# Kernel optimization log

Measured on AMD Instinct MI355X. Metric: run time of the kernel, lower is better.

The kernel has to match this reference:

```python
import jax, jax.numpy as jnp
import numpy as np

ITERS = 20
EPS = 1e-6

def setup_inputs() -> dict:
    key = jax.random.key(0)
    logits = jax.random.normal(key, (128, 64, 64, 64), dtype=jnp.float32)
    return {"logits": logits}

def reference(logits) -> jnp.ndarray:
    # Per-(H,W) matrix: stabilized exp over rows, then 20 Sinkhorn iterations.
    x = logits.astype(jnp.float32)
    # row-wise max (over W, last axis), matching tl.max(x, axis=1)
    x = jnp.exp(x - jnp.max(x, axis=-1, keepdims=True))

    def body(i, x):
        row_sum = jnp.sum(x, axis=-1, keepdims=True)   # sum over W
        x = x / (row_sum + EPS)
        col_sum = jnp.sum(x, axis=-2, keepdims=True)   # sum over H
        x = x / (col_sum + EPS)
        return x

    x = jax.lax.fori_loop(0, ITERS, body, x)
    return x
```

## Files before the change

### kernel.cpp

```cpp
#include <hip/hip_runtime.h>


static constexpr int   kIters = 20;
static constexpr float kEps   = 1e-6f;

__device__ __forceinline__ float RLf(float x, int l) {
    return __int_as_float(__builtin_amdgcn_readlane(__float_as_int(x), l));
}

__global__ __launch_bounds__(256, 4) void sinkhorn64_2m4(const float* __restrict__ in,
                                                         float* __restrict__ out) {
    __shared__ float xb0[2][2][64];
    __shared__ float xb1[2][2][64];
    const int tid  = threadIdx.x;
    const int wid  = tid >> 6;
    const int p    = wid >> 1;
    const int h    = wid & 1;
    const int lane = tid & 63;
    const int c    = (lane + 32 * h) & 63;
    const long m   = (long)blockIdx.x * 2 + p;
    const float* __restrict__ A = in  + m * 4096;
    float* __restrict__ O       = out + m * 4096;

    float cK[32];
#pragma unroll
    for (int i = 0; i < 32; ++i) cK[i] = A[((32 * h + i) << 6) + lane];

    float rK[32];
#pragma unroll
    for (int k4 = 0; k4 < 8; ++k4) {
        const float4 f = *reinterpret_cast<const float4*>(A + (lane << 6) + 32 * h + (k4 << 2));
        rK[4 * k4 + 0] = f.x; rK[4 * k4 + 1] = f.y;
        rK[4 * k4 + 2] = f.z; rK[4 * k4 + 3] = f.w;
    }

    float pm = rK[0];
#pragma unroll
    for (int k = 1; k < 32; ++k) pm = fmaxf(pm, rK[k]);
    xb0[p][h][lane] = pm;
    __syncthreads();
    const float mx  = fmaxf(pm, xb0[p][1 - h][lane]);
    const float mxr = fmaxf(xb0[p][0][c], xb0[p][1][c]);

#pragma unroll
    for (int k = 0; k < 32; ++k) rK[k] = __expf(rK[k] - mx);
#pragma unroll
    for (int i = 0; i < 32; ++i) cK[i] = __expf(cK[i] - RLf(mxr, i));

    float ur = 1.0f, vr = 1.0f;

#pragma unroll 1
    for (int it = 0; it < kIters; ++it) {
        float a0 = 0.f, a1 = 0.f, a2 = 0.f, a3 = 0.f;
#pragma unroll
        for (int k = 0; k < 32; k += 4) {
            a0 = fmaf(RLf(vr, k + 0), rK[k + 0], a0);
            a1 = fmaf(RLf(vr, k + 1), rK[k + 1], a1);
            a2 = fmaf(RLf(vr, k + 2), rK[k + 2], a2);
            a3 = fmaf(RLf(vr, k + 3), rK[k + 3], a3);
        }
        xb1[p][h][lane] = (a0 + a1) + (a2 + a3);
        __syncthreads();
        const float w = xb1[p][0][c] + xb1[p][1][c];
        ur = ur * __builtin_amdgcn_rcpf(fmaf(ur, w, kEps));

        float b0 = 0.f, b1 = 0.f, b2 = 0.f, b3 = 0.f;
#pragma unroll
        for (int i = 0; i < 32; i += 4) {
            b0 = fmaf(RLf(ur, i + 0), cK[i + 0], b0);
            b1 = fmaf(RLf(ur, i + 1), cK[i + 1], b1);
            b2 = fmaf(RLf(ur, i + 2), cK[i + 2], b2);
            b3 = fmaf(RLf(ur, i + 3), cK[i + 3], b3);
        }
        xb0[p][h][lane] = (b0 + b1) + (b2 + b3);
        __syncthreads();
        const float t = xb0[p][0][c] + xb0[p][1][c];
        vr = vr * __builtin_amdgcn_rcpf(fmaf(vr, t, kEps));
    }

    xb1[p][h][lane] = vr;
    __syncthreads();
    const float vfin = xb1[p][0][lane];

#pragma unroll
    for (int i = 0; i < 32; ++i) {
        O[((32 * h + i) << 6) + lane] = RLf(ur, i) * cK[i] * vfin;
    }
}

extern "C" void kernel_launch(void* const* d_in, const int* in_sizes, int n_in,
                              void* d_out, int out_size, void* d_ws, size_t ws_size,
                              hipStream_t stream) {
    const float* in = (const float*)d_in[0];
    float* out      = (float*)d_out;
    sinkhorn64_2m4<<<4096, 256, 0, stream>>>(in, out);
}
```

Before: 87.91 us.

## Store Sinkhorn kernel and scaling vectors in packed fp16 using fdot2

Converts the exponentiated matrix (row and column copies) and the u/v scaling vectors to packed half2 and computes the matrix-vector sums with v_dot2 fp16 instructions that accumulate in fp32. This halves register use for the kernel matrix and the number of readlane and FMA instructions per iteration. It also drops the minBlocks launch bound so occupancy is chosen by register use. The cost is fp16 precision on the matrix entries and on the iterated scalings, which may exceed the accuracy tolerance, and fp16 can underflow for small exp values.

Measured after the change: 117.7 us. 1.34x slower.

```diff
diff --git a/kernel.cpp b/kernel.cpp
--- a/kernel.cpp
+++ b/kernel.cpp
@@ -4,12 +4,22 @@
 static constexpr int   kIters = 20;
 static constexpr float kEps   = 1e-6f;
 
+typedef _Float16 h2 __attribute__((ext_vector_type(2)));
+
 __device__ __forceinline__ float RLf(float x, int l) {
     return __int_as_float(__builtin_amdgcn_readlane(__float_as_int(x), l));
 }
+__device__ __forceinline__ h2 RLh2(h2 x, int l) {
+    int bits;
+    __builtin_memcpy(&bits, &x, 4);
+    int r = __builtin_amdgcn_readlane(bits, l);
+    h2 out;
+    __builtin_memcpy(&out, &r, 4);
+    return out;
+}
 
-__global__ __launch_bounds__(256, 4) void sinkhorn64_2m4(const float* __restrict__ in,
-                                                         float* __restrict__ out) {
+__global__ __launch_bounds__(256) void sinkhorn64_h2(const float* __restrict__ in,
+                                                     float* __restrict__ out) {
     __shared__ float xb0[2][2][64];
     __shared__ float xb1[2][2][64];
     const int tid  = threadIdx.x;
@@ -17,74 +27,100 @@
     const int p    = wid >> 1;
     const int h    = wid & 1;
     const int lane = tid & 63;
-    const int c    = (lane + 32 * h) & 63;
+    const int pl   = lane & 31;
     const long m   = (long)blockIdx.x * 2 + p;
     const float* __restrict__ A = in  + m * 4096;
     float* __restrict__ O       = out + m * 4096;
 
-    float cK[32];
-#pragma unroll
-    for (int i = 0; i < 32; ++i) cK[i] = A[((32 * h + i) << 6) + lane];
-
-    float rK[32];
+    float rKf[32];
 #pragma unroll
     for (int k4 = 0; k4 < 8; ++k4) {
         const float4 f = *reinterpret_cast<const float4*>(A + (lane << 6) + 32 * h + (k4 << 2));
-        rK[4 * k4 + 0] = f.x; rK[4 * k4 + 1] = f.y;
-        rK[4 * k4 + 2] = f.z; rK[4 * k4 + 3] = f.w;
+        rKf[4 * k4 + 0] = f.x; rKf[4 * k4 + 1] = f.y;
+        rKf[4 * k4 + 2] = f.z; rKf[4 * k4 + 3] = f.w;
+    }
+    float pm = rKf[0];
+#pragma unroll
+    for (int k = 1; k < 32; ++k) pm = fmaxf(pm, rKf[k]);
+    xb0[p][h][lane] = pm;
+    __syncthreads();
+    const float mx = fmaxf(pm, xb0[p][1 - h][lane]);
+
+    h2 rH[16];
+#pragma unroll
+    for (int t = 0; t < 16; ++t) {
+        rH[t].x = (_Float16)__expf(rKf[2 * t + 0] - mx);
+        rH[t].y = (_Float16)__expf(rKf[2 * t + 1] - mx);
     }
 
-    float pm = rK[0];
+    h2 cH[16];
 #pragma unroll
-    for (int k = 1; k < 32; ++k) pm = fmaxf(pm, rK[k]);
-    xb0[p][h][lane] = pm;
-    __syncthreads();
-    const float mx  = fmaxf(pm, xb0[p][1 - h][lane]);
-    const float mxr = fmaxf(xb0[p][0][c], xb0[p][1][c]);
+    for (int t = 0; t < 16; ++t) {
+        const float x0 = A[((32 * h + 2 * t + 0) << 6) + lane];
+        const float x1 = A[((32 * h + 2 * t + 1) << 6) + lane];
+        cH[t].x = (_Float16)__expf(x0 - RLf(mx, 32 * h + 2 * t + 0));
+        cH[t].y = (_Float16)__expf(x1 - RLf(mx, 32 * h + 2 * t + 1));
+    }
 
-#pragma unroll
-    for (int k = 0; k < 32; ++k) rK[k] = __expf(rK[k] - mx);
-#pragma unroll
-    for (int i = 0; i < 32; ++i) cK[i] = __expf(cK[i] - RLf(mxr, i));
-
-    float ur = 1.0f, vr = 1.0f;
+    h2 up; up.x = (_Float16)1.0f; up.y = (_Float16)1.0f;
+    h2 vp = up;
+    const int rlbase = 16 * h;
 
 #pragma unroll 1
     for (int it = 0; it < kIters; ++it) {
-        float a0 = 0.f, a1 = 0.f, a2 = 0.f, a3 = 0.f;
+        {
+            float a0 = 0.f, a1 = 0.f, a2 = 0.f, a3 = 0.f;
 #pragma unroll
-        for (int k = 0; k < 32; k += 4) {
-            a0 = fmaf(RLf(vr, k + 0), rK[k + 0], a0);
-            a1 = fmaf(RLf(vr, k + 1), rK[k + 1], a1);
-            a2 = fmaf(RLf(vr, k + 2), rK[k + 2], a2);
-            a3 = fmaf(RLf(vr, k + 3), rK[k + 3], a3);
+            for (int t = 0; t < 16; t += 4) {
+                a0 = __builtin_amdgcn_fdot2(rH[t + 0], RLh2(vp, rlbase + t + 0), a0, false);
+                a1 = __builtin_amdgcn_fdot2(rH[t + 1], RLh2(vp, rlbase + t + 1), a1, false);
+                a2 = __builtin_amdgcn_fdot2(rH[t + 2], RLh2(vp, rlbase + t + 2), a2, false);
+                a3 = __builtin_amdgcn_fdot2(rH[t + 3], RLh2(vp, rlbase + t + 3), a3, false);
+            }
+            xb1[p][h][lane] = (a0 + a1) + (a2 + a3);
         }
-        xb1[p][h][lane] = (a0 + a1) + (a2 + a3);
         __syncthreads();
-        const float w = xb1[p][0][c] + xb1[p][1][c];
-        ur = ur * __builtin_amdgcn_rcpf(fmaf(ur, w, kEps));
+        {
+            const float2 a = *reinterpret_cast<const float2*>(&xb1[p][0][2 * pl]);
+            const float2 b = *reinterpret_cast<const float2*>(&xb1[p][1][2 * pl]);
+            float u0 = (float)up.x, u1 = (float)up.y;
+            u0 = u0 * __builtin_amdgcn_rcpf(fmaf(u0, a.x + b.x, kEps));
+            u1 = u1 * __builtin_amdgcn_rcpf(fmaf(u1, a.y + b.y, kEps));
+            up.x = (_Float16)u0; up.y = (_Float16)u1;
+        }
 
-        float b0 = 0.f, b1 = 0.f, b2 = 0.f, b3 = 0.f;
+        {
+            float a0 = 0.f, a1 = 0.f, a2 = 0.f, a3 = 0.f;
 #pragma unroll
-        for (int i = 0; i < 32; i += 4) {
-            b0 = fmaf(RLf(ur, i + 0), cK[i + 0], b0);
-            b1 = fmaf(RLf(ur, i + 1), cK[i + 1], b1);
-            b2 = fmaf(RLf(ur, i + 2), cK[i + 2], b2);
-            b3 = fmaf(RLf(ur, i + 3), cK[i + 3], b3);
+            for (int t = 0; t < 16; t += 4) {
+                a0 = __builtin_amdgcn_fdot2(cH[t + 0], RLh2(up, rlbase + t + 0), a0, false);
+                a1 = __builtin_amdgcn_fdot2(cH[t + 1], RLh2(up, rlbase + t + 1), a1, false);
+                a2 = __builtin_amdgcn_fdot2(cH[t + 2], RLh2(up, rlbase + t + 2), a2, false);
+                a3 = __builtin_amdgcn_fdot2(cH[t + 3], RLh2(up, rlbase + t + 3), a3, false);
+            }
+            xb0[p][h][lane] = (a0 + a1) + (a2 + a3);
         }
-        xb0[p][h][lane] = (b0 + b1) + (b2 + b3);
         __syncthreads();
-        const float t = xb0[p][0][c] + xb0[p][1][c];
-        vr = vr * __builtin_amdgcn_rcpf(fmaf(vr, t, kEps));
+        {
+            const float2 a = *reinterpret_cast<const float2*>(&xb0[p][0][2 * pl]);
+            const float2 b = *reinterpret_cast<const float2*>(&xb0[p][1][2 * pl]);
+            float v0 = (float)vp.x, v1 = (float)vp.y;
+            v0 = v0 * __builtin_amdgcn_rcpf(fmaf(v0, a.x + b.x, kEps));
+            v1 = v1 * __builtin_amdgcn_rcpf(fmaf(v1, a.y + b.y, kEps));
+            vp.x = (_Float16)v0; vp.y = (_Float16)v1;
+        }
     }
 
-    xb1[p][h][lane] = vr;
     __syncthreads();
-    const float vfin = xb1[p][0][lane];
+    reinterpret_cast<h2*>(&xb0[p][0][0])[pl] = vp;
+    __syncthreads();
+    const float vf = (float)reinterpret_cast<const _Float16*>(&xb0[p][0][0])[lane];
 
 #pragma unroll
-    for (int i = 0; i < 32; ++i) {
-        O[((32 * h + i) << 6) + lane] = RLf(ur, i) * cK[i] * vfin;
+    for (int t = 0; t < 16; ++t) {
+        const h2 u2 = RLh2(up, rlbase + t);
+        O[((32 * h + 2 * t + 0) << 6) + lane] = (float)u2.x * (float)cH[t].x * vf;
+        O[((32 * h + 2 * t + 1) << 6) + lane] = (float)u2.y * (float)cH[t].y * vf;
     }
 }
 
@@ -93,5 +129,5 @@
                               hipStream_t stream) {
     const float* in = (const float*)d_in[0];
     float* out      = (float*)d_out;
-    sinkhorn64_2m4<<<4096, 256, 0, stream>>>(in, out);
+    sinkhorn64_h2<<<4096, 256, 0, stream>>>(in, out);
 }
```

## Hand-write Sinkhorn loop in inline asm with packed FP32 FMAs

Applied to the files above, without the earlier changes.

Replaces the compiler-generated 20-iteration Sinkhorn loop with an inline assembly block. It broadcasts scaling factors through v_readlane into SGPR pairs and accumulates with v_pk_fma_f32, which handles two matrix entries per instruction and halves the FMA instruction count. The two partial sums are kept as float2 pairs in LDS and reduced after the barrier with four ds_read_b32. The risks are hardcoded SGPR clobbers, hand-inserted s_nop hazard padding, and dropping the occupancy hint in launch_bounds.

Measured after the change: 93.02 us. +5.8%, slower.

```diff
diff --git a/kernel.cpp b/kernel.cpp
--- a/kernel.cpp
+++ b/kernel.cpp
@@ -1,17 +1,17 @@
 #include <hip/hip_runtime.h>
 
 
-static constexpr int   kIters = 20;
-static constexpr float kEps   = 1e-6f;
+static constexpr float kEps = 1e-6f;
 
 __device__ __forceinline__ float RLf(float x, int l) {
     return __int_as_float(__builtin_amdgcn_readlane(__float_as_int(x), l));
 }
 
-__global__ __launch_bounds__(256, 4) void sinkhorn64_2m4(const float* __restrict__ in,
-                                                         float* __restrict__ out) {
-    __shared__ float xb0[2][2][64];
-    __shared__ float xb1[2][2][64];
+__global__ __launch_bounds__(256) void sinkhorn64_asm2(const float* __restrict__ in,
+                                                       float* __restrict__ out) {
+    __shared__ float2 xw[2][2][64];
+    __shared__ float2 xt[2][2][64];
+    __shared__ float  mbuf[2][2][64];
     const int tid  = threadIdx.x;
     const int wid  = tid >> 6;
     const int p    = wid >> 1;
@@ -22,69 +22,179 @@
     const float* __restrict__ A = in  + m * 4096;
     float* __restrict__ O       = out + m * 4096;
 
-    float cK[32];
-#pragma unroll
-    for (int i = 0; i < 32; ++i) cK[i] = A[((32 * h + i) << 6) + lane];
-
-    float rK[32];
+    float cKf[32];
+#pragma unroll
+    for (int i = 0; i < 32; ++i) cKf[i] = A[((32 * h + i) << 6) + lane];
+    float rKf[32];
 #pragma unroll
     for (int k4 = 0; k4 < 8; ++k4) {
         const float4 f = *reinterpret_cast<const float4*>(A + (lane << 6) + 32 * h + (k4 << 2));
-        rK[4 * k4 + 0] = f.x; rK[4 * k4 + 1] = f.y;
-        rK[4 * k4 + 2] = f.z; rK[4 * k4 + 3] = f.w;
+        rKf[4 * k4 + 0] = f.x; rKf[4 * k4 + 1] = f.y;
+        rKf[4 * k4 + 2] = f.z; rKf[4 * k4 + 3] = f.w;
     }
 
-    float pm = rK[0];
-#pragma unroll
-    for (int k = 1; k < 32; ++k) pm = fmaxf(pm, rK[k]);
-    xb0[p][h][lane] = pm;
+    float pm = rKf[0];
+#pragma unroll
+    for (int k = 1; k < 32; ++k) pm = fmaxf(pm, rKf[k]);
+    mbuf[p][h][lane] = pm;
     __syncthreads();
-    const float mx  = fmaxf(pm, xb0[p][1 - h][lane]);
-    const float mxr = fmaxf(xb0[p][0][c], xb0[p][1][c]);
-
-#pragma unroll
-    for (int k = 0; k < 32; ++k) rK[k] = __expf(rK[k] - mx);
-#pragma unroll
-    for (int i = 0; i < 32; ++i) cK[i] = __expf(cK[i] - RLf(mxr, i));
+    const float mx  = fmaxf(pm, mbuf[p][1 - h][lane]);
+    const float mxr = fmaxf(mbuf[p][0][c], mbuf[p][1][c]);
+
+    float2 rK2[16], cK2[16];
+#pragma unroll
+    for (int t = 0; t < 16; ++t) {
+        rK2[t].x = __expf(rKf[2 * t + 0] - mx);
+        rK2[t].y = __expf(rKf[2 * t + 1] - mx);
+        cK2[t].x = __expf(cKf[2 * t + 0] - RLf(mxr, 2 * t + 0));
+        cK2[t].y = __expf(cKf[2 * t + 1] - RLf(mxr, 2 * t + 1));
+    }
 
     float ur = 1.0f, vr = 1.0f;
-
-#pragma unroll 1
-    for (int it = 0; it < kIters; ++it) {
-        float a0 = 0.f, a1 = 0.f, a2 = 0.f, a3 = 0.f;
-#pragma unroll
-        for (int k = 0; k < 32; k += 4) {
-            a0 = fmaf(RLf(vr, k + 0), rK[k + 0], a0);
-            a1 = fmaf(RLf(vr, k + 1), rK[k + 1], a1);
-            a2 = fmaf(RLf(vr, k + 2), rK[k + 2], a2);
-            a3 = fmaf(RLf(vr, k + 3), rK[k + 3], a3);
-        }
-        xb1[p][h][lane] = (a0 + a1) + (a2 + a3);
-        __syncthreads();
-        const float w = xb1[p][0][c] + xb1[p][1][c];
-        ur = ur * __builtin_amdgcn_rcpf(fmaf(ur, w, kEps));
-
-        float b0 = 0.f, b1 = 0.f, b2 = 0.f, b3 = 0.f;
-#pragma unroll
-        for (int i = 0; i < 32; i += 4) {
-            b0 = fmaf(RLf(ur, i + 0), cK[i + 0], b0);
-            b1 = fmaf(RLf(ur, i + 1), cK[i + 1], b1);
-            b2 = fmaf(RLf(ur, i + 2), cK[i + 2], b2);
-            b3 = fmaf(RLf(ur, i + 3), cK[i + 3], b3);
-        }
-        xb0[p][h][lane] = (b0 + b1) + (b2 + b3);
-        __syncthreads();
-        const float t = xb0[p][0][c] + xb0[p][1][c];
-        vr = vr * __builtin_amdgcn_rcpf(fmaf(vr, t, kEps));
-    }
-
-    xb1[p][h][lane] = vr;
+    const float epsv = kEps;
+
+    const unsigned wa = (unsigned)(size_t)&xw[p][h][lane];
+    const unsigned ra = (unsigned)(size_t)&xw[p][0][c];
+    const unsigned wb = (unsigned)(size_t)&xt[p][h][lane];
+    const unsigned rb = (unsigned)(size_t)&xt[p][0][c];
+
+    float2 a0, a1, a2, a3;
+    float  t0, t1, t2, t3;
+
+    asm volatile(
+        "s_movk_i32 s68, 20\n"
+        "1:\n"
+        "v_readlane_b32 s36, %[vr], 0\n"  "v_readlane_b32 s37, %[vr], 1\n"
+        "v_readlane_b32 s38, %[vr], 2\n"  "v_readlane_b32 s39, %[vr], 3\n"
+        "v_readlane_b32 s40, %[vr], 4\n"  "v_readlane_b32 s41, %[vr], 5\n"
+        "v_readlane_b32 s42, %[vr], 6\n"  "v_readlane_b32 s43, %[vr], 7\n"
+        "v_readlane_b32 s44, %[vr], 8\n"  "v_readlane_b32 s45, %[vr], 9\n"
+        "v_readlane_b32 s46, %[vr], 10\n" "v_readlane_b32 s47, %[vr], 11\n"
+        "v_readlane_b32 s48, %[vr], 12\n" "v_readlane_b32 s49, %[vr], 13\n"
+        "v_readlane_b32 s50, %[vr], 14\n" "v_readlane_b32 s51, %[vr], 15\n"
+        "v_readlane_b32 s52, %[vr], 16\n" "v_readlane_b32 s53, %[vr], 17\n"
+        "v_readlane_b32 s54, %[vr], 18\n" "v_readlane_b32 s55, %[vr], 19\n"
+        "v_readlane_b32 s56, %[vr], 20\n" "v_readlane_b32 s57, %[vr], 21\n"
+        "v_readlane_b32 s58, %[vr], 22\n" "v_readlane_b32 s59, %[vr], 23\n"
+        "v_readlane_b32 s60, %[vr], 24\n" "v_readlane_b32 s61, %[vr], 25\n"
+        "v_readlane_b32 s62, %[vr], 26\n" "v_readlane_b32 s63, %[vr], 27\n"
+        "v_readlane_b32 s64, %[vr], 28\n" "v_readlane_b32 s65, %[vr], 29\n"
+        "v_readlane_b32 s66, %[vr], 30\n" "v_readlane_b32 s67, %[vr], 31\n"
+        "v_pk_mul_f32 %[a0], s[36:37], %[r0]\n"
+        "v_pk_mul_f32 %[a1], s[38:39], %[r1]\n"
+        "v_pk_mul_f32 %[a2], s[40:41], %[r2]\n"
+        "v_pk_mul_f32 %[a3], s[42:43], %[r3]\n"
+        "v_pk_fma_f32 %[a0], s[44:45], %[r4], %[a0]\n"
+        "v_pk_fma_f32 %[a1], s[46:47], %[r5], %[a1]\n"
+        "v_pk_fma_f32 %[a2], s[48:49], %[r6], %[a2]\n"
+        "v_pk_fma_f32 %[a3], s[50:51], %[r7], %[a3]\n"
+        "v_pk_fma_f32 %[a0], s[52:53], %[r8], %[a0]\n"
+        "v_pk_fma_f32 %[a1], s[54:55], %[r9], %[a1]\n"
+        "v_pk_fma_f32 %[a2], s[56:57], %[r10], %[a2]\n"
+        "v_pk_fma_f32 %[a3], s[58:59], %[r11], %[a3]\n"
+        "v_pk_fma_f32 %[a0], s[60:61], %[r12], %[a0]\n"
+        "v_pk_fma_f32 %[a1], s[62:63], %[r13], %[a1]\n"
+        "v_pk_fma_f32 %[a2], s[64:65], %[r14], %[a2]\n"
+        "v_pk_fma_f32 %[a3], s[66:67], %[r15], %[a3]\n"
+        "v_pk_add_f32 %[a0], %[a0], %[a1]\n"
+        "v_pk_add_f32 %[a2], %[a2], %[a3]\n"
+        "v_pk_add_f32 %[a0], %[a0], %[a2]\n"
+        "ds_write_b64 %[wa], %[a0]\n"
+        "s_waitcnt lgkmcnt(0)\n"
+        "s_barrier\n"
+        "ds_read_b32 %[t0], %[ra] offset:0\n"
+        "ds_read_b32 %[t1], %[ra] offset:4\n"
+        "ds_read_b32 %[t2], %[ra] offset:512\n"
+        "ds_read_b32 %[t3], %[ra] offset:516\n"
+        "s_waitcnt lgkmcnt(0)\n"
+        "v_add_f32 %[t0], %[t0], %[t1]\n"
+        "v_add_f32 %[t2], %[t2], %[t3]\n"
+        "v_add_f32 %[t0], %[t0], %[t2]\n"
+        "v_fma_f32 %[t1], %[ur], %[t0], %[eps]\n"
+        "v_rcp_f32 %[t1], %[t1]\n"
+        "s_nop 1\n"
+        "v_mul_f32 %[ur], %[ur], %[t1]\n"
+        "s_nop 1\n"
+        "v_readlane_b32 s36, %[ur], 0\n"  "v_readlane_b32 s37, %[ur], 1\n"
+        "v_readlane_b32 s38, %[ur], 2\n"  "v_readlane_b32 s39, %[ur], 3\n"
+        "v_readlane_b32 s40, %[ur], 4\n"  "v_readlane_b32 s41, %[ur], 5\n"
+        "v_readlane_b32 s42, %[ur], 6\n"  "v_readlane_b32 s43, %[ur], 7\n"
+        "v_readlane_b32 s44, %[ur], 8\n"  "v_readlane_b32 s45, %[ur], 9\n"
+        "v_readlane_b32 s46, %[ur], 10\n" "v_readlane_b32 s47, %[ur], 11\n"
+        "v_readlane_b32 s48, %[ur], 12\n" "v_readlane_b32 s49, %[ur], 13\n"
+        "v_readlane_b32 s50, %[ur], 14\n" "v_readlane_b32 s51, %[ur], 15\n"
+        "v_readlane_b32 s52, %[ur], 16\n" "v_readlane_b32 s53, %[ur], 17\n"
+        "v_readlane_b32 s54, %[ur], 18\n" "v_readlane_b32 s55, %[ur], 19\n"
+        "v_readlane_b32 s56, %[ur], 20\n" "v_readlane_b32 s57, %[ur], 21\n"
+        "v_readlane_b32 s58, %[ur], 22\n" "v_readlane_b32 s59, %[ur], 23\n"
+        "v_readlane_b32 s60, %[ur], 24\n" "v_readlane_b32 s61, %[ur], 25\n"
+        "v_readlane_b32 s62, %[ur], 26\n" "v_readlane_b32 s63, %[ur], 27\n"
+        "v_readlane_b32 s64, %[ur], 28\n" "v_readlane_b32 s65, %[ur], 29\n"
+        "v_readlane_b32 s66, %[ur], 30\n" "v_readlane_b32 s67, %[ur], 31\n"
+        "v_pk_mul_f32 %[a0], s[36:37], %[c0]\n"
+        "v_pk_mul_f32 %[a1], s[38:39], %[c1]\n"
+        "v_pk_mul_f32 %[a2], s[40:41], %[c2]\n"
+        "v_pk_mul_f32 %[a3], s[42:43], %[c3]\n"
+        "v_pk_fma_f32 %[a0], s[44:45], %[c4], %[a0]\n"
+        "v_pk_fma_f32 %[a1], s[46:47], %[c5], %[a1]\n"
+        "v_pk_fma_f32 %[a2], s[48:49], %[c6], %[a2]\n"
+        "v_pk_fma_f32 %[a3], s[50:51], %[c7], %[a3]\n"
+        "v_pk_fma_f32 %[a0], s[52:53], %[c8], %[a0]\n"
+        "v_pk_fma_f32 %[a1], s[54:55], %[c9], %[a1]\n"
+        "v_pk_fma_f32 %[a2], s[56:57], %[c10], %[a2]\n"
+        "v_pk_fma_f32 %[a3], s[58:59], %[c11], %[a3]\n"
+        "v_pk_fma_f32 %[a0], s[60:61], %[c12], %[a0]\n"
+        "v_pk_fma_f32 %[a1], s[62:63], %[c13], %[a1]\n"
+        "v_pk_fma_f32 %[a2], s[64:65], %[c14], %[a2]\n"
+        "v_pk_fma_f32 %[a3], s[66:67], %[c15], %[a3]\n"
+        "v_pk_add_f32 %[a0], %[a0], %[a1]\n"
+        "v_pk_add_f32 %[a2], %[a2], %[a3]\n"
+        "v_pk_add_f32 %[a0], %[a0], %[a2]\n"
+        "ds_write_b64 %[wb], %[a0]\n"
+        "s_waitcnt lgkmcnt(0)\n"
+        "s_barrier\n"
+        "ds_read_b32 %[t0], %[rb] offset:0\n"
+        "ds_read_b32 %[t1], %[rb] offset:4\n"
+        "ds_read_b32 %[t2], %[rb] offset:512\n"
+        "ds_read_b32 %[t3], %[rb] offset:516\n"
+        "s_waitcnt lgkmcnt(0)\n"
+        "v_add_f32 %[t0], %[t0], %[t1]\n"
+        "v_add_f32 %[t2], %[t2], %[t3]\n"
+        "v_add_f32 %[t0], %[t0], %[t2]\n"
+        "v_fma_f32 %[t1], %[vr], %[t0], %[eps]\n"
+        "v_rcp_f32 %[t1], %[t1]\n"
+        "s_nop 1\n"
+        "v_mul_f32 %[vr], %[vr], %[t1]\n"
+        "s_sub_u32 s68, s68, 1\n"
+        "s_cmp_lg_u32 s68, 0\n"
+        "s_cbranch_scc1 1b\n"
+        : [ur] "+v"(ur), [vr] "+v"(vr),
+          [a0] "=&v"(a0), [a1] "=&v"(a1), [a2] "=&v"(a2), [a3] "=&v"(a3),
+          [t0] "=&v"(t0), [t1] "=&v"(t1), [t2] "=&v"(t2), [t3] "=&v"(t3)
+        : [r0] "v"(rK2[0]),  [r1] "v"(rK2[1]),  [r2] "v"(rK2[2]),  [r3] "v"(rK2[3]),
+          [r4] "v"(rK2[4]),  [r5] "v"(rK2[5]),  [r6] "v"(rK2[6]),  [r7] "v"(rK2[7]),
+          [r8] "v"(rK2[8]),  [r9] "v"(rK2[9]),  [r10] "v"(rK2[10]), [r11] "v"(rK2[11]),
+          [r12] "v"(rK2[12]), [r13] "v"(rK2[13]), [r14] "v"(rK2[14]), [r15] "v"(rK2[15]),
+          [c0] "v"(cK2[0]),  [c1] "v"(cK2[1]),  [c2] "v"(cK2[2]),  [c3] "v"(cK2[3]),
+          [c4] "v"(cK2[4]),  [c5] "v"(cK2[5]),  [c6] "v"(cK2[6]),  [c7] "v"(cK2[7]),
+          [c8] "v"(cK2[8]),  [c9] "v"(cK2[9]),  [c10] "v"(cK2[10]), [c11] "v"(cK2[11]),
+          [c12] "v"(cK2[12]), [c13] "v"(cK2[13]), [c14] "v"(cK2[14]), [c15] "v"(cK2[15]),
+          [wa] "v"(wa), [ra] "v"(ra), [wb] "v"(wb), [rb] "v"(rb), [eps] "v"(epsv)
+        : "s36","s37","s38","s39","s40","s41","s42","s43",
+          "s44","s45","s46","s47","s48","s49","s50","s51",
+          "s52","s53","s54","s55","s56","s57","s58","s59",
+          "s60","s61","s62","s63","s64","s65","s66","s67","s68",
+          "scc","memory");
+
     __syncthreads();
-    const float vfin = xb1[p][0][lane];
-
-#pragma unroll
-    for (int i = 0; i < 32; ++i) {
-        O[((32 * h + i) << 6) + lane] = RLf(ur, i) * cK[i] * vfin;
+    mbuf[p][h][lane] = vr;
+    __syncthreads();
+    const float vfin = mbuf[p][0][lane];
+
+#pragma unroll
+    for (int t = 0; t < 16; ++t) {
+        O[((32 * h + 2 * t + 0) << 6) + lane] = RLf(ur, 2 * t + 0) * cK2[t].x * vfin;
+        O[((32 * h + 2 * t + 1) << 6) + lane] = RLf(ur, 2 * t + 1) * cK2[t].y * vfin;
     }
 }
 
@@ -93,5 +203,5 @@
                               hipStream_t stream) {
     const float* in = (const float*)d_in[0];
     float* out      = (float*)d_out;
-    sinkhorn64_2m4<<<4096, 256, 0, stream>>>(in, out);
+    sinkhorn64_asm2<<<4096, 256, 0, stream>>>(in, out);
 }
```
